# Optimization experiments

Hardware: AMD Instinct MI355X
Metric: run time of the kernel (lower is better)

Reference implementation:

```python
import jax, jax.numpy as jnp
import numpy as np

T, B, I, H = 512, 128, 512, 1024


def setup_inputs() -> dict:
    key = jax.random.key(0)
    ks = jax.random.split(key, 9)
    stdv = 1.0 / np.sqrt(H).astype(np.float32)
    u = lambda k, shape: jax.random.uniform(k, shape, jnp.float32, -stdv, stdv)
    return {
        "x": jax.random.normal(ks[0], (T, B, I), jnp.float32),
        "Wf": u(ks[1], (H, H + I)), "bf": u(ks[2], (H,)),
        "Wi": u(ks[3], (H, H + I)), "bi": u(ks[4], (H,)),
        "Wc": u(ks[5], (H, H + I)), "bc": u(ks[6], (H,)),
        "Wo": u(ks[7], (H, H + I)), "bo": u(ks[8], (H,)),
    }


def reference(x, Wf, bf, Wi, bi, Wc, bc, Wo, bo):
    # Single-layer unidirectional LSTM (colah equations), scan over time.
    hidden = Wf.shape[0]
    batch = x.shape[1]

    def step(carry, xt):
        h, c = carry
        z = jnp.concatenate([h, xt], axis=-1)          # (B, H+I)
        f = jax.nn.sigmoid(z @ Wf.T + bf)              # forget gate
        i = jax.nn.sigmoid(z @ Wi.T + bi)              # input gate
        c_tilde = jnp.tanh(z @ Wc.T + bc)              # candidate cell
        o = jax.nn.sigmoid(z @ Wo.T + bo)              # output gate
        c_new = f * c + i * c_tilde
        h_new = o * jnp.tanh(c_new)
        return (h_new, c_new), h_new

    h0 = jnp.zeros((batch, hidden), x.dtype)
    c0 = jnp.zeros((batch, hidden), x.dtype)
    (_, _), hs = jax.lax.scan(step, (h0, c0), x)       # hs: (T, B, H)
    return hs
```

## Files before the change

kernel.cpp:

```cpp
#include <hip/hip_runtime.h>
#include <hip/hip_fp16.h>

#define TSTEPS 512
#define NB 128
#define NI 512
#define HID 1024
#define NWGS 256

typedef _Float16 __attribute__((ext_vector_type(8))) half8;
typedef float __attribute__((ext_vector_type(16))) floatx16;
typedef float __attribute__((ext_vector_type(4))) float4v;
typedef unsigned __attribute__((ext_vector_type(4))) uint4v;

#define WPACK_OFF 0
#define HB0_OFF   12582912
#define HB1_OFF   12845056
#define BAR_OFF   13107200

#define LDS_PBUF  98304
#define LDS_HSH   135168
#define LDS_TOTAL 137728

__device__ __forceinline__ short f2h(float f) {
  _Float16 h = (_Float16)f;
  return *reinterpret_cast<short*>(&h);
}

__device__ __forceinline__ half8 pack8(float4v a, float4v b) {
  half8 r;
  r[0] = (_Float16)a[0]; r[1] = (_Float16)a[1]; r[2] = (_Float16)a[2]; r[3] = (_Float16)a[3];
  r[4] = (_Float16)b[0]; r[5] = (_Float16)b[1]; r[6] = (_Float16)b[2]; r[7] = (_Float16)b[3];
  return r;
}

__device__ __forceinline__ float sigf(float x) { return 1.f / (1.f + __expf(-x)); }

__device__ __forceinline__ uint4v cp_load4(const unsigned* p) {
  uint4v v;
  asm volatile("global_load_dwordx4 %0, %1, off sc0 sc1" : "=v"(v) : "v"(p) : "memory");
  asm volatile("s_waitcnt vmcnt(0)" ::: "memory");
  return v;
}
__device__ __forceinline__ void cp_store(unsigned* p, unsigned v) {
  asm volatile("global_store_dword %0, %1, off sc0 sc1" :: "v"(p), "v"(v) : "memory");
}

__global__ void pack_w(const float* __restrict__ Wf, const float* __restrict__ Wi,
                       const float* __restrict__ Wc, const float* __restrict__ Wo,
                       _Float16* __restrict__ wpack) {
  int idx = blockIdx.x * 256 + threadIdx.x;
  if (idx >= 128 * 96 * 64) return;
  int lane = idx & 63;
  int rest = idx >> 6;
  int kt = rest % 96;
  int hs = rest / 96;
  int n = lane & 31, q = lane >> 5;
  int j = n >> 2, g = n & 3;
  int row = hs * 8 + j;
  int k = kt * 16 + q * 8;
  const float* W = (g == 0) ? Wf : (g == 1) ? Wi : (g == 2) ? Wc : Wo;
  const float* src = W + (size_t)row * 1536 + k;
  _Float16* dst = wpack + (size_t)idx * 8;
  #pragma unroll
  for (int e = 0; e < 8; e++) dst[e] = (_Float16)src[e];
}

__global__ void zero_h(unsigned* __restrict__ hb0, unsigned* __restrict__ bar) {
  int i = blockIdx.x * 256 + threadIdx.x;
  if (i < 65536)
    __hip_atomic_store(&hb0[i], 0u, __ATOMIC_RELAXED, __HIP_MEMORY_SCOPE_SYSTEM);
  if (i < 2048)
    __hip_atomic_store(&bar[i], 0u, __ATOMIC_RELAXED, __HIP_MEMORY_SCOPE_SYSTEM);
}

__global__ void __launch_bounds__(256, 1)
lstm_main(const float* __restrict__ x,
          const float* __restrict__ bfv, const float* __restrict__ biv,
          const float* __restrict__ bcv, const float* __restrict__ bov,
          const _Float16* __restrict__ wpack,
          _Float16* __restrict__ hb0, _Float16* __restrict__ hb1,
          unsigned* __restrict__ bar, float* __restrict__ out) {
  extern __shared__ char lds[];
  short* wlds = (short*)lds;
  float* pbuf = (float*)(lds + LDS_PBUF);
  float* hshare = (float*)(lds + LDS_HSH);

  const int tid = threadIdx.x;
  const int lane = tid & 63;
  const int wv = tid >> 6;
  const int hs = blockIdx.x & 127;
  const int mh = blockIdx.x >> 7;

  {
    const uint4* src = (const uint4*)wpack + (size_t)hs * 6144;
    uint4* dst = (uint4*)wlds;
    #pragma unroll
    for (int i = 0; i < 24; i++) dst[i * 256 + tid] = src[i * 256 + tid];
  }

  const int rj = tid & 7;
  const int rm4 = tid >> 3;
  float rbias[4] = {0.f, 0.f, 0.f, 0.f};
  float cstate[4] = {0.f, 0.f, 0.f, 0.f};
  if (tid < 128) {
    int hg = hs * 8 + rj;
    rbias[0] = bfv[hg]; rbias[1] = biv[hg]; rbias[2] = bcv[hg]; rbias[3] = bov[hg];
  }

  const int n32 = lane & 31;
  const int q = lane >> 5;

  unsigned* myslot = bar + ((blockIdx.x >> 2) * 32 + (blockIdx.x & 3));
  const unsigned* pline = bar + (((mh * 128 + wv * 32) >> 2) + (lane & 7)) * 32;

  __syncthreads();

  for (int t = 0; t < TSTEPS; t++) {
    const _Float16* hrd = (t & 1) ? hb1 : hb0;
    _Float16* hwr = (t & 1) ? hb0 : hb1;

    floatx16 acc0, acc1;
    #pragma unroll
    for (int i = 0; i < 16; i++) { acc0[i] = 0.f; acc1[i] = 0.f; }

    {
      const float* xbase = x + (size_t)t * NB * NI;
      const int r0 = (mh * 2 + 0) * 32 + n32;
      #pragma unroll
      for (int kk = 0; kk < 8; kk++) {
        int xt = wv * 8 + kk;
        half8 bfrag = *(const half8*)(wlds + ((64 + xt) * 64 + lane) * 8);
        const float* xs = xbase + xt * 16 + q * 8;
        float4v xa0 = *(const float4v*)(xs + (size_t)r0 * NI);
        float4v xb0 = *(const float4v*)(xs + (size_t)r0 * NI + 4);
        float4v xa1 = *(const float4v*)(xs + (size_t)(r0 + 32) * NI);
        float4v xb1 = *(const float4v*)(xs + (size_t)(r0 + 32) * NI + 4);
        acc0 = __builtin_amdgcn_mfma_f32_32x32x16_f16(pack8(xa0, xb0), bfrag, acc0, 0, 0, 0);
        acc1 = __builtin_amdgcn_mfma_f32_32x32x16_f16(pack8(xa1, xb1), bfrag, acc1, 0, 0, 0);
      }
    }

    if (t > 0) {
      const unsigned need = (unsigned)t;
      for (;;) {
        int ok = 1;
        if (lane < 8) {
          uint4v v = cp_load4(pline);
          ok = (v[0] >= need) & (v[1] >= need) & (v[2] >= need) & (v[3] >= need);
        }
        if (__all(ok)) break;
        __builtin_amdgcn_s_sleep(1);
      }
    }

    {
      const char* hp = (const char*)hrd + ((size_t)mh << 17);
      #pragma unroll
      for (int ph = 0; ph < 2; ph++) {
        uint4v wa[8], wb[8];
        #pragma unroll
        for (int kk = 0; kk < 8; kk++) {
          int ht = wv * 16 + ph * 8 + kk;
          const char* base = hp + (((ht * 2 + q) << 10) | (n32 << 4));
          asm volatile("global_load_dwordx4 %0, %1, off sc0 sc1"
                       : "=v"(wa[kk]) : "v"(base));
          asm volatile("global_load_dwordx4 %0, %1, off offset:512 sc0 sc1"
                       : "=v"(wb[kk]) : "v"(base));
        }
        #pragma unroll
        for (int kk = 0; kk < 8; kk++) {
          int ht = wv * 16 + ph * 8 + kk;
          half8 bfrag = *(const half8*)(wlds + (ht * 64 + lane) * 8);
          asm volatile("s_waitcnt vmcnt(%0)" :: "i"(14 - 2 * kk) : "memory");
          __builtin_amdgcn_sched_barrier(0);
          union { uint4v u; half8 h; } ua, ub;
          ua.u = wa[kk]; ub.u = wb[kk];
          acc0 = __builtin_amdgcn_mfma_f32_32x32x16_f16(ua.h, bfrag, acc0, 0, 0, 0);
          acc1 = __builtin_amdgcn_mfma_f32_32x32x16_f16(ub.h, bfrag, acc1, 0, 0, 0);
        }
      }
    }

    {
      float* b0 = pbuf + ((wv * 2 + 0) * 32 + n32) * 36 + q * 4;
      float* b1 = pbuf + ((wv * 2 + 1) * 32 + n32) * 36 + q * 4;
      #pragma unroll
      for (int rg = 0; rg < 4; rg++) {
        float4v v0 = {acc0[rg * 4 + 0], acc0[rg * 4 + 1], acc0[rg * 4 + 2], acc0[rg * 4 + 3]};
        float4v v1 = {acc1[rg * 4 + 0], acc1[rg * 4 + 1], acc1[rg * 4 + 2], acc1[rg * 4 + 3]};
        *(float4v*)(b0 + rg * 8) = v0;
        *(float4v*)(b1 + rg * 8) = v1;
      }
    }
    __syncthreads();

    if (tid < 128) {
      const int mt = rm4 >> 3;
      const int mb = (rm4 & 7) * 4;
      float4v s[4];
      #pragma unroll
      for (int g = 0; g < 4; g++) {
        const float* p = pbuf + (mt * 32 + rj * 4 + g) * 36 + mb;
        float4v a = *(const float4v*)(p);
        a += *(const float4v*)(p + 1 * 2 * 32 * 36);
        a += *(const float4v*)(p + 2 * 2 * 32 * 36);
        a += *(const float4v*)(p + 3 * 2 * 32 * 36);
        s[g] = a;
      }
      #pragma unroll
      for (int r = 0; r < 4; r++) {
        float fg = sigf(s[0][r] + rbias[0]);
        float ig = sigf(s[1][r] + rbias[1]);
        float cg = tanhf(s[2][r] + rbias[2]);
        float og = sigf(s[3][r] + rbias[3]);
        float cn = fg * cstate[r] + ig * cg;
        cstate[r] = cn;
        hshare[(rm4 * 4 + r) * 10 + rj] = og * tanhf(cn);
      }
    }
    __syncthreads();

    {
      const int ml = tid >> 2;
      const int j0 = (tid & 3) * 2;
      float h0 = hshare[ml * 10 + j0];
      float h1 = hshare[ml * 10 + j0 + 1];

      unsigned u = ((unsigned)(unsigned short)f2h(h1) << 16) | (unsigned)(unsigned short)f2h(h0);
      unsigned* dst = (unsigned*)((char*)hwr + (((mh * 128 + hs) << 10))) + tid;
      cp_store(dst, u);

      const int mg = mh * 64 + ml;
      const int hg = hs * 8 + j0;
      *(float2*)(out + ((size_t)t * NB + mg) * HID + hg) = make_float2(h0, h1);
    }

    if (t < TSTEPS - 1) {
      __syncthreads();
      if (tid == 0) cp_store(myslot, (unsigned)(t + 1));
    }
  }
}

extern "C" void kernel_launch(void* const* d_in, const int* in_sizes, int n_in,
                              void* d_out, int out_size, void* d_ws, size_t ws_size,
                              hipStream_t stream) {
  const float* x   = (const float*)d_in[0];
  const float* Wf  = (const float*)d_in[1];
  const float* bf_ = (const float*)d_in[2];
  const float* Wi  = (const float*)d_in[3];
  const float* bi_ = (const float*)d_in[4];
  const float* Wc  = (const float*)d_in[5];
  const float* bc_ = (const float*)d_in[6];
  const float* Wo  = (const float*)d_in[7];
  const float* bo_ = (const float*)d_in[8];
  float* out = (float*)d_out;

  char* ws = (char*)d_ws;
  _Float16* wpack = (_Float16*)(ws + WPACK_OFF);
  _Float16* hb0   = (_Float16*)(ws + HB0_OFF);
  _Float16* hb1   = (_Float16*)(ws + HB1_OFF);
  unsigned* bar   = (unsigned*)(ws + BAR_OFF);

  pack_w<<<3072, 256, 0, stream>>>(Wf, Wi, Wc, Wo, wpack);
  zero_h<<<257, 256, 0, stream>>>((unsigned*)hb0, bar);

  hipFuncSetAttribute(reinterpret_cast<const void*>(lstm_main),
                      hipFuncAttributeMaxDynamicSharedMemorySize, LDS_TOTAL);

  void* args[] = {(void*)&x, (void*)&bf_, (void*)&bi_, (void*)&bc_, (void*)&bo_,
                  (void*)&wpack, (void*)&hb0, (void*)&hb1, (void*)&bar, (void*)&out};
  hipLaunchCooperativeKernel(reinterpret_cast<void*>(lstm_main),
                             dim3(NWGS), dim3(256), args, LDS_TOTAL, stream);
}
```

Measured before the change: 4.106 ms.

## Prepack x to fp16 MFMA layout and shorten the h-publish barrier path

A new pre-kernel converts all of x into fp16 in the MFMA fragment layout. Each timestep can then load A-fragments directly instead of reading fp32 rows and converting them inside the recurrent loop. The h write-back is reduced to one wave issuing dwordx4 stores, which then signal the barrier slot right after its own stores complete. This drops one __syncthreads per step from the critical inter-workgroup path. The changes add a 64 MB workspace pass and depend on ws_size, falling back to the old path if the workspace is too small.

```diff
diff --git a/kernel.cpp b/kernel.cpp
--- a/kernel.cpp
+++ b/kernel.cpp
@@ -16,14 +16,19 @@
 #define HB0_OFF   12582912
 #define HB1_OFF   12845056
 #define BAR_OFF   13107200
+#define XPK_OFF   13115392
+#define XPK_NEED  ((size_t)XPK_OFF + (size_t)67108864)
 
 #define LDS_PBUF  98304
 #define LDS_HSH   135168
-#define LDS_TOTAL 137728
+#define LDS_TOTAL 137984
 
 __device__ __forceinline__ short f2h(float f) {
   _Float16 h = (_Float16)f;
   return *reinterpret_cast<short*>(&h);
+}
+__device__ __forceinline__ unsigned pack2(float a, float b) {
+  return ((unsigned)(unsigned short)f2h(b) << 16) | (unsigned)(unsigned short)f2h(a);
 }
 
 __device__ __forceinline__ half8 pack8(float4v a, float4v b) {
@@ -43,6 +48,9 @@
 }
 __device__ __forceinline__ void cp_store(unsigned* p, unsigned v) {
   asm volatile("global_store_dword %0, %1, off sc0 sc1" :: "v"(p), "v"(v) : "memory");
+}
+__device__ __forceinline__ void cp_store4(unsigned* p, uint4v v) {
+  asm volatile("global_store_dwordx4 %0, %1, off sc0 sc1" :: "v"(p), "v"(v) : "memory");
 }
 
 __global__ void pack_w(const float* __restrict__ Wf, const float* __restrict__ Wi,
@@ -65,6 +73,21 @@
   for (int e = 0; e < 8; e++) dst[e] = (_Float16)src[e];
 }
 
+__global__ void pack_x(const float* __restrict__ x, _Float16* __restrict__ xpk) {
+  int idx = blockIdx.x * 256 + threadIdx.x;
+  int lane = idx & 63;
+  int rest = idx >> 6;
+  int xt = rest & 31;
+  rest >>= 5;
+  int mt = rest & 3;
+  int t = rest >> 2;
+  int n32 = lane & 31, q = lane >> 5;
+  const float* src = x + ((size_t)t * NB + mt * 32 + n32) * NI + xt * 16 + q * 8;
+  _Float16* dst = xpk + (size_t)idx * 8;
+  #pragma unroll
+  for (int e = 0; e < 8; e++) dst[e] = (_Float16)src[e];
+}
+
 __global__ void zero_h(unsigned* __restrict__ hb0, unsigned* __restrict__ bar) {
   int i = blockIdx.x * 256 + threadIdx.x;
   if (i < 65536)
@@ -77,7 +100,8 @@
 lstm_main(const float* __restrict__ x,
           const float* __restrict__ bfv, const float* __restrict__ biv,
           const float* __restrict__ bcv, const float* __restrict__ bov,
-          const _Float16* __restrict__ wpack,
+          const _Float16* __restrict__ wpack, const _Float16* __restrict__ xpk,
+          int xp_en,
           _Float16* __restrict__ hb0, _Float16* __restrict__ hb1,
           unsigned* __restrict__ bar, float* __restrict__ out) {
   extern __shared__ char lds[];
@@ -123,7 +147,18 @@
     #pragma unroll
     for (int i = 0; i < 16; i++) { acc0[i] = 0.f; acc1[i] = 0.f; }
 
-    {
+    if (xp_en) {
+      const _Float16* xp = xpk + (((size_t)t * 4 + mh * 2) * 32) * 64 * 8;
+      #pragma unroll
+      for (int kk = 0; kk < 8; kk++) {
+        int xt = wv * 8 + kk;
+        half8 bfrag = *(const half8*)(wlds + ((64 + xt) * 64 + lane) * 8);
+        half8 a0 = *(const half8*)(xp + ((size_t)(0 * 32 + xt) * 64 + lane) * 8);
+        half8 a1 = *(const half8*)(xp + ((size_t)(1 * 32 + xt) * 64 + lane) * 8);
+        acc0 = __builtin_amdgcn_mfma_f32_32x32x16_f16(a0, bfrag, acc0, 0, 0, 0);
+        acc1 = __builtin_amdgcn_mfma_f32_32x32x16_f16(a1, bfrag, acc1, 0, 0, 0);
+      }
+    } else {
       const float* xbase = x + (size_t)t * NB * NI;
       const int r0 = (mh * 2 + 0) * 32 + n32;
       #pragma unroll
@@ -215,29 +250,33 @@
         float og = sigf(s[3][r] + rbias[3]);
         float cn = fg * cstate[r] + ig * cg;
         cstate[r] = cn;
-        hshare[(rm4 * 4 + r) * 10 + rj] = og * tanhf(cn);
+        hshare[(rm4 * 4 + r) * 11 + rj] = og * tanhf(cn);
       }
     }
     __syncthreads();
+
+    if (t < TSTEPS - 1 && tid < 64) {
+      float v0 = hshare[tid * 11 + 0], v1 = hshare[tid * 11 + 1];
+      float v2 = hshare[tid * 11 + 2], v3 = hshare[tid * 11 + 3];
+      float v4 = hshare[tid * 11 + 4], v5 = hshare[tid * 11 + 5];
+      float v6 = hshare[tid * 11 + 6], v7 = hshare[tid * 11 + 7];
+      uint4v u;
+      u[0] = pack2(v0, v1); u[1] = pack2(v2, v3);
+      u[2] = pack2(v4, v5); u[3] = pack2(v6, v7);
+      unsigned* dst = (unsigned*)((char*)hwr + (((mh * 128 + hs) << 10))) + tid * 4;
+      cp_store4(dst, u);
+      asm volatile("s_waitcnt vmcnt(0)" ::: "memory");
+      if (tid == 0) cp_store(myslot, (unsigned)(t + 1));
+    }
 
     {
       const int ml = tid >> 2;
       const int j0 = (tid & 3) * 2;
-      float h0 = hshare[ml * 10 + j0];
-      float h1 = hshare[ml * 10 + j0 + 1];
-
-      unsigned u = ((unsigned)(unsigned short)f2h(h1) << 16) | (unsigned)(unsigned short)f2h(h0);
-      unsigned* dst = (unsigned*)((char*)hwr + (((mh * 128 + hs) << 10))) + tid;
-      cp_store(dst, u);
-
+      float h0 = hshare[ml * 11 + j0];
+      float h1 = hshare[ml * 11 + j0 + 1];
       const int mg = mh * 64 + ml;
       const int hg = hs * 8 + j0;
       *(float2*)(out + ((size_t)t * NB + mg) * HID + hg) = make_float2(h0, h1);
-    }
-
-    if (t < TSTEPS - 1) {
-      __syncthreads();
-      if (tid == 0) cp_store(myslot, (unsigned)(t + 1));
     }
   }
 }
@@ -261,15 +300,19 @@
   _Float16* hb0   = (_Float16*)(ws + HB0_OFF);
   _Float16* hb1   = (_Float16*)(ws + HB1_OFF);
   unsigned* bar   = (unsigned*)(ws + BAR_OFF);
+  _Float16* xpk   = (_Float16*)(ws + XPK_OFF);
+  int xp_en = (ws_size >= XPK_NEED) ? 1 : 0;
 
   pack_w<<<3072, 256, 0, stream>>>(Wf, Wi, Wc, Wo, wpack);
+  if (xp_en) pack_x<<<16384, 256, 0, stream>>>(x, xpk);
   zero_h<<<257, 256, 0, stream>>>((unsigned*)hb0, bar);
 
   hipFuncSetAttribute(reinterpret_cast<const void*>(lstm_main),
                       hipFuncAttributeMaxDynamicSharedMemorySize, LDS_TOTAL);
 
   void* args[] = {(void*)&x, (void*)&bf_, (void*)&bi_, (void*)&bc_, (void*)&bo_,
-                  (void*)&wpack, (void*)&hb0, (void*)&hb1, (void*)&bar, (void*)&out};
+                  (void*)&wpack, (void*)&xpk, (void*)&xp_en,
+                  (void*)&hb0, (void*)&hb1, (void*)&bar, (void*)&out};
   hipLaunchCooperativeKernel(reinterpret_cast<void*>(lstm_main),
                              dim3(NWGS), dim3(256), args, LDS_TOTAL, stream);
 }
```

Result: slower. 4.711 ms (+14.7%).
